# Kernel optimization log

Hardware: AMD Instinct MI355X
Metric: run time of the kernel (lower is better)

Reference implementation:

```python
import jax, jax.numpy as jnp
import numpy as np
from jax.scipy.linalg import expm

NUM_WIRES = 10
DIM = 2 ** NUM_WIRES  # 1024, statevector dimension
N_GATES = 8


def setup_inputs() -> dict:
    key = jax.random.key(0)
    kf, kg, kt = jax.random.split(key, 3)
    # feature to be amplitude-embedded (AmplitudeEmbedding pads with 0 and L2-normalizes)
    feature = jax.random.normal(kf, (DIM,), jnp.float32)
    # dense Hermitian gate generators (real symmetric), one per selected gate
    A = jax.random.normal(kg, (N_GATES, DIM, DIM), jnp.float32) / np.float32(np.sqrt(DIM))
    gens = 0.5 * (A + jnp.swapaxes(A, -1, -2))
    # learned parameters theta, shape (n_gates, 1) as in the flax module
    theta = jax.random.normal(kt, (N_GATES, 1), jnp.float32)
    return {"feature": feature, "theta": theta, "gens": gens}


def reference(feature, theta, gens):
    # AmplitudeEmbedding: pad (no-op here, len == DIM) then L2-normalize -> complex state
    psi = (feature / jnp.linalg.norm(feature)).astype(jnp.complex64)  # [DIM]

    def apply_gate(psi, gate):
        G, t = gate  # G: [DIM, DIM] complex, t: scalar complex
        U = expm(-1j * t * G)          # qml.exp(-1j * theta * gen)
        return U @ psi, None

    gens_c = gens.astype(jnp.complex64)
    thetas_c = theta[:, 0].astype(jnp.complex64)
    psi, _ = jax.lax.scan(apply_gate, psi, (gens_c, thetas_c))
    # qml.probs(wires=all): Born-rule probabilities over the full register
    return jnp.real(psi * jnp.conj(psi)).astype(jnp.float32)  # [DIM]
```

## Files before the change

kernel.cpp:

```cpp
#include <hip/hip_runtime.h>

#define DIM   1024
#define NG    8
#define NBLK  128
#define TPB   512
#define WAVES (TPB / 64)
#define ROWS_PER_BLK WAVES
#define SCALE    1.45f
#define INVSCALE (1.0f / SCALE)
#define CTOL  5e-3f
#define KMAX  12
#define FSTRIDE 16

typedef unsigned long long u64;
union f2u { float2 f; u64 u; };


__global__ __launch_bounds__(TPB) void qsim_kernel(
    const float* __restrict__ feat,
    const float* __restrict__ theta,
    const float* __restrict__ gens,
    float*       __restrict__ out,
    u64*         __restrict__ vbuf0,
    u64*         __restrict__ vbuf1,
    unsigned*    __restrict__ flags)
{
  const int tid  = threadIdx.x;
  const int lane = tid & 63;
  const int wid  = tid >> 6;
  const int bid  = blockIdx.x;
  const int row  = bid * ROWS_PER_BLK + wid;

  __shared__ float2   smemV[DIM];
  __shared__ float    red[WAVES];
  __shared__ unsigned wdone;
  __shared__ unsigned ready;

  float a[16];
  {
    const float* Gr = gens + (size_t)row * DIM;
    #pragma unroll
    for (int p = 0; p < 16; ++p) a[p] = Gr[p * 64 + lane];
  }

  if (tid == 0) { wdone = 0; ready = 0; }
  {
    float f0 = feat[tid], f1 = feat[tid + TPB];
    float s = f0 * f0 + f1 * f1;
    #pragma unroll
    for (int mm = 1; mm < 64; mm <<= 1) s += __shfl_xor(s, mm);
    if (lane == 0) red[wid] = s;
  }
  __syncthreads();
  float tot = 0.f;
  #pragma unroll
  for (int i = 0; i < WAVES; ++i) tot += red[i];
  const float inv = 1.0f / sqrtf(tot);

  float pr = feat[row] * inv;
  float pi = 0.f;

  unsigned pub = 0;

  auto pub_store = [&](float sr, float si) {
    u64* dst = ((pub + 1) & 1) ? vbuf1 : vbuf0;
    if (lane == 0) {
      f2u x; x.f = make_float2(sr, si);
      __hip_atomic_store(dst + row, x.u,
                         __ATOMIC_RELAXED, __HIP_MEMORY_SCOPE_AGENT);
    }
  };
  auto pub_commit = [&]() {
    __builtin_amdgcn_sched_barrier(0);
    __builtin_amdgcn_s_waitcnt(0);
    __builtin_amdgcn_sched_barrier(0);
    ++pub;
    if (lane == 0) {
      unsigned old = atomicAdd(&wdone, 1u);
      if (old == WAVES * pub - 1) {
        __hip_atomic_store(flags + bid * FSTRIDE, pub,
                           __ATOMIC_RELAXED, __HIP_MEMORY_SCOPE_AGENT);
      }
    }
  };

  for (int g = 0; g < NG; ++g) {
    const float  th = theta[g];
    const double z  = (double)th * (double)SCALE;
    const double az = fmax(fabs(z), 1e-6);
    const float  sg = (th < 0.f) ? -1.f : 1.f;

    double bv[19];
    bv[18] = 1e-30;
    bv[17] = (36.0 / az) * 1e-30;
    #pragma unroll
    for (int k = 17; k >= 1; --k)
      bv[k - 1] = (2.0 * (double)k / az) * bv[k] - bv[k + 1];
    double S = bv[0];
    #pragma unroll
    for (int k = 2; k <= 18; k += 2) S += 2.0 * bv[k];
    const double invS = 1.0 / S;

    float jc[KMAX + 2];
    #pragma unroll
    for (int k = 0; k <= KMAX + 1; ++k) jc[k] = (float)(bv[k] * invS);

    int m = KMAX; bool found = false;
    #pragma unroll
    for (int k = 1; k <= KMAX; ++k) {
      if (!found && (double)(k + 1) > az &&
          fabs(bv[k + 1] * invS) < (double)CTOL) { m = k; found = true; }
    }

    float accr = jc[0] * pr, acci = jc[0] * pi;
    float wm1r = pr, wm1i = pi, wm2r = 0.f, wm2i = 0.f;
    float anext[16];

    #pragma unroll
    for (int k = 1; k <= KMAX; ++k) {
      if (k > m) break;

      float2 v[16];
      if (g == 0 && k == 1) {
        #pragma unroll
        for (int p = 0; p < 16; ++p)
          v[p] = make_float2(feat[p * 64 + lane] * inv, 0.f);
      } else {
        if (wid == 0) {
          unsigned a0 = __hip_atomic_load(flags + lane * FSTRIDE,
                                          __ATOMIC_RELAXED, __HIP_MEMORY_SCOPE_AGENT);
          unsigned b0 = __hip_atomic_load(flags + (lane + 64) * FSTRIDE,
                                          __ATOMIC_RELAXED, __HIP_MEMORY_SCOPE_AGENT);
          unsigned a1 = __hip_atomic_load(flags + lane * FSTRIDE,
                                          __ATOMIC_RELAXED, __HIP_MEMORY_SCOPE_AGENT);
          unsigned b1 = __hip_atomic_load(flags + (lane + 64) * FSTRIDE,
                                          __ATOMIC_RELAXED, __HIP_MEMORY_SCOPE_AGENT);
          unsigned a2 = __hip_atomic_load(flags + lane * FSTRIDE,
                                          __ATOMIC_RELAXED, __HIP_MEMORY_SCOPE_AGENT);
          unsigned b2 = __hip_atomic_load(flags + (lane + 64) * FSTRIDE,
                                          __ATOMIC_RELAXED, __HIP_MEMORY_SCOPE_AGENT);
          unsigned a3 = __hip_atomic_load(flags + lane * FSTRIDE,
                                          __ATOMIC_RELAXED, __HIP_MEMORY_SCOPE_AGENT);
          unsigned b3 = __hip_atomic_load(flags + (lane + 64) * FSTRIDE,
                                          __ATOMIC_RELAXED, __HIP_MEMORY_SCOPE_AGENT);
          for (;;) {
            if (__all((((int)(a0 - pub) >= 0) & ((int)(b0 - pub) >= 0)))) break;
            __builtin_amdgcn_s_sleep(1);
            a0 = a1; b0 = b1; a1 = a2; b1 = b2; a2 = a3; b2 = b3;
            a3 = __hip_atomic_load(flags + lane * FSTRIDE,
                                   __ATOMIC_RELAXED, __HIP_MEMORY_SCOPE_AGENT);
            b3 = __hip_atomic_load(flags + (lane + 64) * FSTRIDE,
                                   __ATOMIC_RELAXED, __HIP_MEMORY_SCOPE_AGENT);
          }
          const u64* vsrc = (pub & 1) ? vbuf1 : vbuf0;
          f2u x[16];
          #pragma unroll
          for (int p = 0; p < 16; ++p)
            x[p].u = __hip_atomic_load(vsrc + p * 64 + lane,
                                       __ATOMIC_RELAXED, __HIP_MEMORY_SCOPE_AGENT);
          #pragma unroll
          for (int p = 0; p < 16; ++p) smemV[p * 64 + lane] = x[p].f;
          __hip_atomic_store(&ready, pub, __ATOMIC_RELEASE,
                             __HIP_MEMORY_SCOPE_WORKGROUP);
          #pragma unroll
          for (int p = 0; p < 16; ++p) v[p] = x[p].f;
        } else {
          while ((int)(__hip_atomic_load(&ready, __ATOMIC_ACQUIRE,
                                         __HIP_MEMORY_SCOPE_WORKGROUP) - pub) < 0) {
            __builtin_amdgcn_s_sleep(1);
          }
          #pragma unroll
          for (int p = 0; p < 16; ++p) v[p] = smemV[p * 64 + lane];
        }
      }

      float yr = 0.f, yi = 0.f;
      #pragma unroll
      for (int p = 0; p < 16; ++p) {
        yr = fmaf(a[p], v[p].x, yr);
        yi = fmaf(a[p], v[p].y, yi);
      }
      #pragma unroll
      for (int mm = 1; mm < 64; mm <<= 1) {
        yr += __shfl_xor(yr, mm);
        yi += __shfl_xor(yi, mm);
      }

      const float ur = yr * INVSCALE;
      const float ui = yi * INVSCALE;
      const float wkr = (k == 1) ? ur : fmaf(2.f, ur, -wm2r);
      const float wki = (k == 1) ? ui : fmaf(2.f, ui, -wm2i);

      const bool last = (k == m);
      if (!last) pub_store(wkr, wki);

      {
        const float j2  = 2.f * jc[k];
        const float sj2 = sg * j2;
        if ((k & 3) == 0) {
          accr = fmaf(j2, wkr, accr);
          acci = fmaf(j2, wki, acci);
        } else if ((k & 3) == 1) {
          accr = fmaf( sj2, wki, accr);
          acci = fmaf(-sj2, wkr, acci);
        } else if ((k & 3) == 2) {
          accr = fmaf(-j2, wkr, accr);
          acci = fmaf(-j2, wki, acci);
        } else {
          accr = fmaf(-sj2, wki, accr);
          acci = fmaf( sj2, wkr, acci);
        }
      }

      if (!last) pub_commit();

      if (k == 1 && g < NG - 1) {
        const float* Gr = gens + (size_t)(g + 1) * DIM * DIM
                               + (size_t)row * DIM;
        #pragma unroll
        for (int p = 0; p < 16; ++p) anext[p] = Gr[p * 64 + lane];
      }

      if (last) {
        if (g < NG - 1) {
          pub_store(accr, acci);
          pub_commit();
        }
      } else {
        wm2r = wm1r; wm2i = wm1i;
        wm1r = wkr;  wm1i = wki;
      }
    }

    if (g < NG - 1) {
      #pragma unroll
      for (int p = 0; p < 16; ++p) a[p] = anext[p];
    }
    pr = accr; pi = acci;
  }

  if (lane == 0) out[row] = pr * pr + pi * pi;
}

extern "C" void kernel_launch(void* const* d_in, const int* in_sizes, int n_in,
                              void* d_out, int out_size, void* d_ws, size_t ws_size,
                              hipStream_t stream) {
  const float* feat  = (const float*)d_in[0];
  const float* theta = (const float*)d_in[1];
  const float* gens  = (const float*)d_in[2];
  float* out = (float*)d_out;

  unsigned* flags = (unsigned*)d_ws;
  u64* vbuf0 = (u64*)((char*)d_ws + 8192);
  u64* vbuf1 = (u64*)((char*)d_ws + 8192 + (size_t)DIM * sizeof(u64));

  qsim_kernel<<<dim3(NBLK), dim3(TPB), 0, stream>>>(
      feat, theta, gens, out, vbuf0, vbuf1, flags);
}
```

Baseline: 155.5 us.

## Replace per-block flags with sequence-tagged vector words and block-aggregated publish

```diff
diff --git a/kernel.cpp b/kernel.cpp
--- a/kernel.cpp
+++ b/kernel.cpp
@@ -5,16 +5,23 @@
 #define NBLK  128
 #define TPB   512
 #define WAVES (TPB / 64)
-#define ROWS_PER_BLK WAVES
 #define SCALE    1.45f
 #define INVSCALE (1.0f / SCALE)
 #define CTOL  5e-3f
 #define KMAX  12
-#define FSTRIDE 16
+#define SEGW  (2 * WAVES)
 
 typedef unsigned long long u64;
-union f2u { float2 f; u64 u; };
-
+
+
+__device__ __forceinline__ u64 packw(float v, unsigned seq) {
+  union { float f; unsigned u; } c; c.f = v;
+  return ((u64)seq << 32) | (u64)c.u;
+}
+__device__ __forceinline__ float unpackf(u64 x) {
+  union { unsigned u; float f; } c; c.u = (unsigned)x;
+  return c.f;
+}
 
 __global__ __launch_bounds__(TPB) void qsim_kernel(
     const float* __restrict__ feat,
@@ -22,19 +29,21 @@
     const float* __restrict__ gens,
     float*       __restrict__ out,
     u64*         __restrict__ vbuf0,
-    u64*         __restrict__ vbuf1,
-    unsigned*    __restrict__ flags)
+    u64*         __restrict__ vbuf1)
 {
   const int tid  = threadIdx.x;
   const int lane = tid & 63;
   const int wid  = tid >> 6;
   const int bid  = blockIdx.x;
-  const int row  = bid * ROWS_PER_BLK + wid;
+  const int row  = bid * WAVES + wid;
 
   __shared__ float2   smemV[DIM];
+  __shared__ float2   smemPub[WAVES];
   __shared__ float    red[WAVES];
   __shared__ unsigned wdone;
   __shared__ unsigned ready;
+  float* smemVf   = (float*)smemV;
+  float* smemPubF = (float*)smemPub;
 
   float a[16];
   {
@@ -61,27 +70,33 @@
   float pi = 0.f;
 
   unsigned pub = 0;
-
-  auto pub_store = [&](float sr, float si) {
-    u64* dst = ((pub + 1) & 1) ? vbuf1 : vbuf0;
-    if (lane == 0) {
-      f2u x; x.f = make_float2(sr, si);
-      __hip_atomic_store(dst + row, x.u,
-                         __ATOMIC_RELAXED, __HIP_MEMORY_SCOPE_AGENT);
-    }
+  bool  pend_anext = false;
+  int   gnext = 0;
+  float anext[16];
+
+  auto publish = [&](float sr, float si) {
+    if (lane == 0) smemPub[wid] = make_float2(sr, si);
+    asm volatile("s_waitcnt lgkmcnt(0)" ::: "memory");
+    unsigned old = 0;
+    if (lane == 0) old = atomicAdd(&wdone, 1u);
+    old = __shfl(old, 0);
+    const unsigned seq = pub + 1;
+    if (old == WAVES * seq - 1) {
+      u64* dst = (seq & 1) ? vbuf1 : vbuf0;
+      if (lane < SEGW) {
+        const float f = smemPubF[lane];
+        __hip_atomic_store(dst + bid * SEGW + lane, packw(f, seq),
+                           __ATOMIC_RELAXED, __HIP_MEMORY_SCOPE_AGENT);
+      }
+    }
+    ++pub;
   };
-  auto pub_commit = [&]() {
-    __builtin_amdgcn_sched_barrier(0);
-    __builtin_amdgcn_s_waitcnt(0);
-    __builtin_amdgcn_sched_barrier(0);
-    ++pub;
-    if (lane == 0) {
-      unsigned old = atomicAdd(&wdone, 1u);
-      if (old == WAVES * pub - 1) {
-        __hip_atomic_store(flags + bid * FSTRIDE, pub,
-                           __ATOMIC_RELAXED, __HIP_MEMORY_SCOPE_AGENT);
-      }
-    }
+
+  auto issue_anext = [&]() {
+    const float* Gr = gens + (size_t)gnext * DIM * DIM + (size_t)row * DIM;
+    #pragma unroll
+    for (int p = 0; p < 16; ++p) anext[p] = Gr[p * 64 + lane];
+    pend_anext = false;
   };
 
   for (int g = 0; g < NG; ++g) {
@@ -114,7 +129,6 @@
 
     float accr = jc[0] * pr, acci = jc[0] * pi;
     float wm1r = pr, wm1i = pi, wm2r = 0.f, wm2i = 0.f;
-    float anext[16];
 
     #pragma unroll
     for (int k = 1; k <= KMAX; ++k) {
@@ -127,43 +141,29 @@
           v[p] = make_float2(feat[p * 64 + lane] * inv, 0.f);
       } else {
         if (wid == 0) {
-          unsigned a0 = __hip_atomic_load(flags + lane * FSTRIDE,
-                                          __ATOMIC_RELAXED, __HIP_MEMORY_SCOPE_AGENT);
-          unsigned b0 = __hip_atomic_load(flags + (lane + 64) * FSTRIDE,
-                                          __ATOMIC_RELAXED, __HIP_MEMORY_SCOPE_AGENT);
-          unsigned a1 = __hip_atomic_load(flags + lane * FSTRIDE,
-                                          __ATOMIC_RELAXED, __HIP_MEMORY_SCOPE_AGENT);
-          unsigned b1 = __hip_atomic_load(flags + (lane + 64) * FSTRIDE,
-                                          __ATOMIC_RELAXED, __HIP_MEMORY_SCOPE_AGENT);
-          unsigned a2 = __hip_atomic_load(flags + lane * FSTRIDE,
-                                          __ATOMIC_RELAXED, __HIP_MEMORY_SCOPE_AGENT);
-          unsigned b2 = __hip_atomic_load(flags + (lane + 64) * FSTRIDE,
-                                          __ATOMIC_RELAXED, __HIP_MEMORY_SCOPE_AGENT);
-          unsigned a3 = __hip_atomic_load(flags + lane * FSTRIDE,
-                                          __ATOMIC_RELAXED, __HIP_MEMORY_SCOPE_AGENT);
-          unsigned b3 = __hip_atomic_load(flags + (lane + 64) * FSTRIDE,
-                                          __ATOMIC_RELAXED, __HIP_MEMORY_SCOPE_AGENT);
+          const u64* vsrc = (pub & 1) ? vbuf1 : vbuf0;
           for (;;) {
-            if (__all((((int)(a0 - pub) >= 0) & ((int)(b0 - pub) >= 0)))) break;
-            __builtin_amdgcn_s_sleep(1);
-            a0 = a1; b0 = b1; a1 = a2; b1 = b2; a2 = a3; b2 = b3;
-            a3 = __hip_atomic_load(flags + lane * FSTRIDE,
-                                   __ATOMIC_RELAXED, __HIP_MEMORY_SCOPE_AGENT);
-            b3 = __hip_atomic_load(flags + (lane + 64) * FSTRIDE,
-                                   __ATOMIC_RELAXED, __HIP_MEMORY_SCOPE_AGENT);
+            u64 x[32];
+            #pragma unroll
+            for (int c = 0; c < 32; ++c)
+              x[c] = __hip_atomic_load(vsrc + c * 64 + lane,
+                                       __ATOMIC_RELAXED, __HIP_MEMORY_SCOPE_AGENT);
+            bool ok = true;
+            #pragma unroll
+            for (int c = 0; c < 32; ++c)
+              ok = ok && ((unsigned)(x[c] >> 32) == pub);
+            if (__all(ok)) {
+              #pragma unroll
+              for (int c = 0; c < 32; ++c) smemVf[c * 64 + lane] = unpackf(x[c]);
+              break;
+            }
+            __builtin_amdgcn_s_sleep(2);
           }
-          const u64* vsrc = (pub & 1) ? vbuf1 : vbuf0;
-          f2u x[16];
-          #pragma unroll
-          for (int p = 0; p < 16; ++p)
-            x[p].u = __hip_atomic_load(vsrc + p * 64 + lane,
-                                       __ATOMIC_RELAXED, __HIP_MEMORY_SCOPE_AGENT);
-          #pragma unroll
-          for (int p = 0; p < 16; ++p) smemV[p * 64 + lane] = x[p].f;
           __hip_atomic_store(&ready, pub, __ATOMIC_RELEASE,
                              __HIP_MEMORY_SCOPE_WORKGROUP);
+          if (pend_anext) issue_anext();
           #pragma unroll
-          for (int p = 0; p < 16; ++p) v[p] = x[p].f;
+          for (int p = 0; p < 16; ++p) v[p] = smemV[p * 64 + lane];
         } else {
           while ((int)(__hip_atomic_load(&ready, __ATOMIC_ACQUIRE,
                                          __HIP_MEMORY_SCOPE_WORKGROUP) - pub) < 0) {
@@ -192,7 +192,7 @@
       const float wki = (k == 1) ? ui : fmaf(2.f, ui, -wm2i);
 
       const bool last = (k == m);
-      if (!last) pub_store(wkr, wki);
+      if (!last) publish(wkr, wki);
 
       {
         const float j2  = 2.f * jc[k];
@@ -212,20 +212,19 @@
         }
       }
 
-      if (!last) pub_commit();
-
       if (k == 1 && g < NG - 1) {
-        const float* Gr = gens + (size_t)(g + 1) * DIM * DIM
-                               + (size_t)row * DIM;
-        #pragma unroll
-        for (int p = 0; p < 16; ++p) anext[p] = Gr[p * 64 + lane];
+        if (wid != 0) {
+          const float* Gr = gens + (size_t)(g + 1) * DIM * DIM
+                                 + (size_t)row * DIM;
+          #pragma unroll
+          for (int p = 0; p < 16; ++p) anext[p] = Gr[p * 64 + lane];
+        } else {
+          pend_anext = true; gnext = g + 1;
+        }
       }
 
       if (last) {
-        if (g < NG - 1) {
-          pub_store(accr, acci);
-          pub_commit();
-        }
+        if (g < NG - 1) publish(accr, acci);
       } else {
         wm2r = wm1r; wm2i = wm1i;
         wm1r = wkr;  wm1i = wki;
@@ -233,6 +232,7 @@
     }
 
     if (g < NG - 1) {
+      if (wid == 0 && pend_anext) issue_anext();
       #pragma unroll
       for (int p = 0; p < 16; ++p) a[p] = anext[p];
     }
@@ -250,10 +250,9 @@
   const float* gens  = (const float*)d_in[2];
   float* out = (float*)d_out;
 
-  unsigned* flags = (unsigned*)d_ws;
-  u64* vbuf0 = (u64*)((char*)d_ws + 8192);
-  u64* vbuf1 = (u64*)((char*)d_ws + 8192 + (size_t)DIM * sizeof(u64));
+  u64* vbuf0 = (u64*)d_ws;
+  u64* vbuf1 = (u64*)((char*)d_ws + (size_t)DIM * 2 * sizeof(u64));
 
   qsim_kernel<<<dim3(NBLK), dim3(TPB), 0, stream>>>(
-      feat, theta, gens, out, vbuf0, vbuf1, flags);
-}
+      feat, theta, gens, out, vbuf0, vbuf1);
+}
```

After: 144.2 us. -7.3%, faster.
